# Optimization experiments

Hardware: AMD Instinct MI355X
Metric: run time of the kernel (lower is better)

Reference implementation:

```python
import jax, jax.numpy as jnp
import numpy as np

T, DM = 2048, 2048
H, KV, D = 16, 2, 128
E, I_MOE, I_SH = 16, 768, 768
TOP_K, N_GROUP, TOPK_GROUP = 4, 4, 2
ROPE_THETA = 1e6
EPS = 1e-5
ROUTED_SCALE = 1.0


def rmsnorm(x, w):
    v = jnp.mean(x * x, axis=-1, keepdims=True)
    return x * jax.lax.rsqrt(v + EPS) * w


def apply_rope(x, pos):
    # partial rotary: first D//2 dims rotated (neox style), rest passthrough
    rd = D // 2
    half = rd // 2
    inv = 1.0 / (ROPE_THETA ** (jnp.arange(0, rd, 2, dtype=jnp.float32) / rd))
    freqs = pos.astype(jnp.float32)[:, None] * inv  # [T, half]
    cos = jnp.cos(freqs)[:, None, :]
    sin = jnp.sin(freqs)[:, None, :]
    x1, x2 = x[..., :half], x[..., half:rd]
    rot = jnp.concatenate([x1 * cos - x2 * sin, x2 * cos + x1 * sin], axis=-1)
    return jnp.concatenate([rot, x[..., rd:]], axis=-1)


def mlp(x, wgu, wd):
    g, u = jnp.split(x @ wgu, 2, axis=-1)
    return (jax.nn.silu(g) * u) @ wd


def attention(x, pos, w_qkv, b_qkv, w_o, q_norm_w, k_norm_w):
    qkv = x @ w_qkv + b_qkv
    q, k, v = jnp.split(qkv, [H * D, H * D + KV * D], axis=-1)
    q = rmsnorm(q.reshape(T, H, D), q_norm_w)
    k = rmsnorm(k.reshape(T, KV, D), k_norm_w)
    v = v.reshape(T, KV, D)
    q = apply_rope(q, pos)
    k = apply_rope(k, pos)
    rep = H // KV
    k = jnp.repeat(k, rep, axis=1)
    v = jnp.repeat(v, rep, axis=1)
    scores = jnp.einsum('thd,shd->hts', q, k) * (D ** -0.5)
    causal = pos[:, None] >= pos[None, :]
    scores = jnp.where(causal[None], scores, jnp.finfo(scores.dtype).min)
    p = jax.nn.softmax(scores, axis=-1)
    o = jnp.einsum('hts,shd->thd', p, v).reshape(T, H * D)
    return o @ w_o


def moe(x, gate_w, gate_bias, shared_wgu, shared_wd, expert_wgu, expert_wd):
    # sigmoid grouped top-k routing with e_score_correction_bias (DeepSeek/GLM style)
    logits = x.astype(jnp.float32) @ gate_w
    scores = jax.nn.sigmoid(logits)
    sb = scores + gate_bias
    g = sb.reshape(T, N_GROUP, E // N_GROUP)
    group_scores = jnp.sum(jax.lax.top_k(g, 2)[0], axis=-1)  # [T, n_group]
    _, gi = jax.lax.top_k(group_scores, TOPK_GROUP)
    gmask = jnp.zeros((T, N_GROUP)).at[jnp.arange(T)[:, None], gi].set(1.0)
    emask = jnp.repeat(gmask, E // N_GROUP, axis=1)
    masked = jnp.where(emask > 0, sb, -jnp.inf)
    _, idx = jax.lax.top_k(masked, TOP_K)  # [T, top_k]
    w = jnp.take_along_axis(scores, idx, axis=1)
    w = w / jnp.sum(w, axis=1, keepdims=True)  # renormalize (norm_topk_prob)
    cw = jnp.zeros((T, E)).at[jnp.arange(T)[:, None], idx].add(w)  # dense combine weights
    gu = jnp.einsum('td,edi->tei', x, expert_wgu)  # [T, E, 2I]
    gt, ut = jnp.split(gu, 2, axis=-1)
    act = jax.nn.silu(gt) * ut * cw[:, :, None]
    routed = jnp.einsum('tei,eid->td', act, expert_wd)
    shared = mlp(x, shared_wgu, shared_wd)
    return routed * ROUTED_SCALE + shared


def setup_inputs() -> dict:
    key = jax.random.key(0)
    ks = jax.random.split(key, 12)
    s = 0.02
    return {
        'positions': jnp.arange(T, dtype=jnp.int32),
        'hidden_states': jax.random.normal(ks[0], (T, DM), jnp.float32),
        'residual': jax.random.normal(ks[1], (T, DM), jnp.float32),
        'ln1_w': jnp.ones((DM,), jnp.float32),
        'ln2_w': jnp.ones((DM,), jnp.float32),
        'w_qkv': jax.random.normal(ks[2], (DM, (H + 2 * KV) * D), jnp.float32) * s,
        'b_qkv': jnp.zeros(((H + 2 * KV) * D,), jnp.float32),
        'w_o': jax.random.normal(ks[3], (H * D, DM), jnp.float32) * s,
        'q_norm_w': jnp.ones((D,), jnp.float32),
        'k_norm_w': jnp.ones((D,), jnp.float32),
        'gate_w': jax.random.normal(ks[4], (DM, E), jnp.float32) * s,
        'gate_bias': jax.random.normal(ks[5], (E,), jnp.float32) * 0.1,
        'shared_wgu': jax.random.normal(ks[6], (DM, 2 * I_SH), jnp.float32) * s,
        'shared_wd': jax.random.normal(ks[7], (I_SH, DM), jnp.float32) * s,
        'expert_wgu': jax.random.normal(ks[8], (E, DM, 2 * I_MOE), jnp.float32) * s,
        'expert_wd': jax.random.normal(ks[9], (E, I_MOE, DM), jnp.float32) * s,
    }


def reference(positions, hidden_states, residual, ln1_w, ln2_w, w_qkv, b_qkv, w_o,
              q_norm_w, k_norm_w, gate_w, gate_bias, shared_wgu, shared_wd,
              expert_wgu, expert_wd):
    # fused add + RMSNorm (residual is not None path)
    residual = hidden_states + residual
    h = rmsnorm(residual, ln1_w)
    h = attention(h, positions, w_qkv, b_qkv, w_o, q_norm_w, k_norm_w)
    residual = h + residual
    h = rmsnorm(residual, ln2_w)
    h = moe(h, gate_w, gate_bias, shared_wgu, shared_wd, expert_wgu, expert_wd)
    return h, residual
```

## Files before the change

kernel.cpp:

```cpp
#include <hip/hip_runtime.h>
#include <stdint.h>
#include <math.h>

#define T_ 2048
#define DM 2048
#define NH 16
#define NKV 2
#define HD 128
#define QKVN 2560
#define NE 16
#define IM 768
#define ISH 768
#define MAXROWS 10240
#define ROWS_ALL 12288
#define NBLK 136
#define SM_SCALE 0.08838834764831845f

typedef __attribute__((ext_vector_type(8))) short short8;
typedef __attribute__((ext_vector_type(4))) float f32x4;

__device__ __forceinline__ float bf2f(unsigned short u){ return __uint_as_float(((unsigned int)u)<<16); }
__device__ __forceinline__ unsigned short f2bf(float f){
  unsigned int u = __float_as_uint(f);
  return (unsigned short)((u + 0x7FFFu + ((u>>16)&1u)) >> 16);
}
__device__ __forceinline__ void split2(float x, unsigned short& hi, unsigned short& lo){
  hi = f2bf(x);
  lo = f2bf(x - bf2f(hi));
}

__device__ __forceinline__ void gload16(const void* g, void* l){
  __builtin_amdgcn_global_load_lds((const __attribute__((address_space(1))) unsigned int*)g,
                                   (__attribute__((address_space(3))) unsigned int*)l, 16, 0, 0);
}

__device__ __forceinline__ int xcd_swz(int bid, int nwg){
  int q = nwg >> 3, r = nwg & 7, x = bid & 7, p = bid >> 3;
  return (x < r ? x*(q+1) : r*(q+1) + (x-r)*q) + p;
}

#define BAR()    asm volatile("s_barrier" ::: "memory")
#define VW(N)    asm volatile("s_waitcnt vmcnt(" #N ")" ::: "memory")
#define LW0()    do{ asm volatile("s_waitcnt lgkmcnt(0)" ::: "memory"); __builtin_amdgcn_sched_barrier(0); }while(0)

template<bool ILV>
__global__ void k_tconv(const float* __restrict__ src, unsigned short* __restrict__ dst,
                        const float* __restrict__ srcS, unsigned short* __restrict__ dstS,
                        int R, int C, size_t sS, size_t sD){
  int z = blockIdx.z;
  if (srcS && z == gridDim.z-1){ src = srcS; dst = dstS; }
  else { src += (size_t)z * sS; dst += (size_t)z * sD; }
  __shared__ float tile[64*65];
  int tid = threadIdx.x;
  int r0 = blockIdx.y*64, c0 = blockIdx.x*64;
  int lr = tid>>4, lc = (tid&15)*4;
  #pragma unroll
  for (int j=0;j<4;j++){
    int row = j*16 + lr;
    float4 v = *(const float4*)&src[(size_t)(r0+row)*C + c0 + lc];
    float* t = &tile[row*65 + lc];
    t[0]=v.x; t[1]=v.y; t[2]=v.z; t[3]=v.w;
  }
  __syncthreads();
  #pragma unroll
  for (int jj=0;jj<2;jj++){
    int slot = jj*256 + tid;
    int c = slot>>3, ro = (slot&7)*8;
    int cg = c0 + c;
    int cd = cg;
    if (ILV){ int b = cg>>3, inner = cg&7; cd = (b<96 ? b*16 : (b-96)*16+8) + inner; }
    short8 o;
    #pragma unroll
    for (int k=0;k<8;k++) o[k] = (short)f2bf(tile[(ro+k)*65 + c]);
    *(short8*)&dst[(size_t)cd*R + r0 + ro] = o;
  }
}

__global__ void k_tconv2(const float* __restrict__ srcA, unsigned short* __restrict__ dhiA,
                         unsigned short* __restrict__ dloA,
                         const float* __restrict__ srcB, unsigned short* __restrict__ dhiB,
                         unsigned short* __restrict__ dloB){
  const float* src; unsigned short* dhi; unsigned short* dlo; int R, C;
  if (blockIdx.z == 0){ src = srcA; dhi = dhiA; dlo = dloA; R = DM; C = QKVN; }
  else {
    if (blockIdx.x >= DM/64) return;
    src = srcB; dhi = dhiB; dlo = dloB; R = DM; C = DM;
  }
  __shared__ float tile[64*65];
  int tid = threadIdx.x;
  int r0 = blockIdx.y*64, c0 = blockIdx.x*64;
  int lr = tid>>4, lc = (tid&15)*4;
  #pragma unroll
  for (int j=0;j<4;j++){
    int row = j*16 + lr;
    float4 v = *(const float4*)&src[(size_t)(r0+row)*C + c0 + lc];
    float* t = &tile[row*65 + lc];
    t[0]=v.x; t[1]=v.y; t[2]=v.z; t[3]=v.w;
  }
  __syncthreads();
  #pragma unroll
  for (int jj=0;jj<2;jj++){
    int slot = jj*256 + tid;
    int c = slot>>3, ro = (slot&7)*8;
    short8 oh, ol;
    #pragma unroll
    for (int k=0;k<8;k++){
      unsigned short h_, l_;
      split2(tile[(ro+k)*65 + c], h_, l_);
      oh[k] = (short)h_; ol[k] = (short)l_;
    }
    size_t o = (size_t)(c0+c)*R + r0 + ro;
    *(short8*)&dhi[o] = oh;
    *(short8*)&dlo[o] = ol;
  }
}

template<bool ROUTE>
__global__ void k_add_rmsnorm(const float* __restrict__ a, const float* __restrict__ b,
                              const float* __restrict__ w, float* __restrict__ resout,
                              unsigned short* __restrict__ ohi, unsigned short* __restrict__ olo,
                              unsigned short* __restrict__ obf,
                              const float* __restrict__ gw, const float* __restrict__ gbias,
                              int* __restrict__ idx4, float* __restrict__ w4){
  int t = blockIdx.x, tid = threadIdx.x;
  const float4* a4 = (const float4*)(a + (size_t)t*DM);
  const float4* b4 = (const float4*)(b + (size_t)t*DM);
  float4 va = a4[tid], vb = b4[tid];
  float4 wa = a4[tid+256], wb = b4[tid+256];
  float4 v0, v1;
  v0.x=va.x+vb.x; v0.y=va.y+vb.y; v0.z=va.z+vb.z; v0.w=va.w+vb.w;
  v1.x=wa.x+wb.x; v1.y=wa.y+wb.y; v1.z=wa.z+wb.z; v1.w=wa.w+wb.w;
  float s = v0.x*v0.x+v0.y*v0.y+v0.z*v0.z+v0.w*v0.w
          + v1.x*v1.x+v1.y*v1.y+v1.z*v1.z+v1.w*v1.w;
  #pragma unroll
  for (int o=32;o;o>>=1) s += __shfl_xor(s,o);
  __shared__ float sm[4];
  if ((tid&63)==0) sm[tid>>6]=s;
  __syncthreads();
  s = sm[0]+sm[1]+sm[2]+sm[3];
  float rs = rsqrtf(s*(1.f/(float)DM) + 1e-5f);
  ((float4*)(resout + (size_t)t*DM))[tid] = v0;
  ((float4*)(resout + (size_t)t*DM))[tid+256] = v1;
  const float4* w4p_ = (const float4*)w;
  float4 w0 = w4p_[tid], w1 = w4p_[tid+256];
  float n[8] = { v0.x*rs*w0.x, v0.y*rs*w0.y, v0.z*rs*w0.z, v0.w*rs*w0.w,
                 v1.x*rs*w1.x, v1.y*rs*w1.y, v1.z*rs*w1.z, v1.w*rs*w1.w };
  if (ohi){
    ushort4 h0,h1,l0,l1;
    split2(n[0],h0.x,l0.x); split2(n[1],h0.y,l0.y); split2(n[2],h0.z,l0.z); split2(n[3],h0.w,l0.w);
    split2(n[4],h1.x,l1.x); split2(n[5],h1.y,l1.y); split2(n[6],h1.z,l1.z); split2(n[7],h1.w,l1.w);
    ((ushort4*)(ohi + (size_t)t*DM))[tid] = h0;
    ((ushort4*)(ohi + (size_t)t*DM))[tid+256] = h1;
    ((ushort4*)(olo + (size_t)t*DM))[tid] = l0;
    ((ushort4*)(olo + (size_t)t*DM))[tid+256] = l1;
  }
  if (obf){
    ushort4 o0 = make_ushort4(f2bf(n[0]),f2bf(n[1]),f2bf(n[2]),f2bf(n[3]));
    ushort4 o1 = make_ushort4(f2bf(n[4]),f2bf(n[5]),f2bf(n[6]),f2bf(n[7]));
    ((ushort4*)(obf + (size_t)t*DM))[tid] = o0;
    ((ushort4*)(obf + (size_t)t*DM))[tid+256] = o1;
  }
  if constexpr (ROUTE){
    __shared__ float xrow[DM];
    __shared__ float red[16][17];
    #pragma unroll
    for (int jj=0;jj<4;jj++) xrow[4*tid+jj] = n[jj];
    #pragma unroll
    for (int jj=0;jj<4;jj++) xrow[1024+4*tid+jj] = n[4+jj];
    __syncthreads();
    int e = tid & 15, grp = tid >> 4;
    float part = 0.f;
    #pragma unroll 8
    for (int c = grp; c < DM; c += 16)
      part += xrow[c] * gw[(size_t)c*16 + e];
    red[grp][e] = part;
    __syncthreads();
    if (tid==0){
      float sc[16], sb[16];
      for (int ee=0;ee<16;ee++){
        float lg = 0.f;
        for (int g2=0;g2<16;g2++) lg += red[g2][ee];
        sc[ee] = 1.f/(1.f+expf(-lg));
        sb[ee] = sc[ee] + gbias[ee];
      }
      float gs[4];
      for (int g=0;g<4;g++){
        float m1=-3.4e38f, m2=-3.4e38f;
        for (int j=0;j<4;j++){
          float v = sb[g*4+j];
          if (v>m1){ m2=m1; m1=v; } else if (v>m2) m2=v;
        }
        gs[g]=m1+m2;
      }
      int g1=0; for (int g=1;g<4;g++) if (gs[g]>gs[g1]) g1=g;
      int g2=-1; for (int g=0;g<4;g++){ if (g==g1) continue; if (g2<0 || gs[g]>gs[g2]) g2=g; }
      float msk[16];
      for (int ee=0;ee<16;ee++){ int g=ee>>2; msk[ee] = (g==g1||g==g2)? sb[ee] : -3.4e38f; }
      int id[4]; float wv[4]; float wsum=0.f;
      for (int s2=0;s2<4;s2++){
        int bb=0; float bv=-3.5e38f;
        for (int ee=0;ee<16;ee++) if (msk[ee]>bv){ bv=msk[ee]; bb=ee; }
        id[s2]=bb; wv[s2]=sc[bb]; wsum+=sc[bb]; msk[bb]=-3.5e38f;
      }
      float invs = 1.f/wsum;
      for (int s2=0;s2<4;s2++){
        idx4[t*4+s2]=id[s2];
        w4[t*4+s2]=wv[s2]*invs;
      }
    }
  }
}

template<bool GATHER, bool ACT>
__global__ __launch_bounds__(256) void k_gemm2(
    const unsigned short* __restrict__ A, const unsigned short* __restrict__ Be,
    const unsigned short* __restrict__ Bsh, unsigned short* __restrict__ C,
    int K, int lda, int ldb, int ldc,
    const int* __restrict__ offs, size_t sBe, const int* __restrict__ tok){
  int nx = gridDim.x;
  int nwg = nx * gridDim.y;
  int wid_ = xcd_swz(blockIdx.x + nx*blockIdx.y, nwg);
  int tN = wid_ % nx, tM = wid_ / nx;
  int rb = tM*128;
  if (rb >= offs[17]) return;
  const unsigned short* B;
  if (rb >= offs[16]) B = Bsh;
  else {
    int e=0;
    for (; e<15; ++e) if (offs[e+1] > rb) break;
    B = Be + (size_t)e*sBe;
  }
  __shared__ __align__(16) unsigned short As[2][4096];
  __shared__ __align__(16) unsigned short Bs[2][4096];
  int tid = threadIdx.x, lane = tid & 63, wwid = tid >> 6;
  int wr = wwid >> 1, wc = wwid & 1;
  const unsigned short* Bb = B + (size_t)tN*128*ldb;

  const unsigned short* Asrc0;
  const unsigned short* Asrc1;
  int r0s = tid>>2, r1s = r0s + 64;
  {
    if (GATHER){
      Asrc0 = A + (size_t)tok[rb + r0s]*lda;
      Asrc1 = A + (size_t)tok[rb + r1s]*lda;
    } else {
      Asrc0 = A + (size_t)(rb + r0s)*lda;
      Asrc1 = A + (size_t)(rb + r1s)*lda;
    }
  }
  int kc = tid&3;
  int sw = (r0s>>1)&3;
  int kcS = (kc ^ sw)*8;

  f32x4 acc[4][4];
  #pragma unroll
  for (int m=0;m<4;m++)
    #pragma unroll
    for (int n=0;n<4;n++) acc[m][n] = (f32x4){0.f,0.f,0.f,0.f};

  auto STAGE = [&](int b, int k0){
    gload16(Asrc0 + k0 + kcS, As[b] + (size_t)tid*8);
    gload16(Asrc1 + k0 + kcS, As[b] + (size_t)(256+tid)*8);
    gload16(Bb + (size_t)r0s*ldb + k0 + kcS, Bs[b] + (size_t)tid*8);
    gload16(Bb + (size_t)r1s*ldb + k0 + kcS, Bs[b] + (size_t)(256+tid)*8);
  };

  int nt = K >> 5, L = nt - 1;
  STAGE(0, 0);
  if (L >= 1) STAGE(1, 32);
  int i15 = lane & 15, g = lane >> 4;
  for (int i=0; i<nt; ++i){
    int cur = i & 1;
    if (i < L) { VW(4); } else { VW(0); }
    BAR();
    short8 af[4], bfr[4];
    #pragma unroll
    for (int m=0;m<4;m++){
      int row = wr*64 + m*16 + i15;
      int geff = g ^ ((row>>1)&3);
      af[m] = *(const short8*)(As[cur] + row*32 + geff*8);
    }
    #pragma unroll
    for (int n=0;n<4;n++){
      int row = wc*64 + n*16 + i15;
      int geff = g ^ ((row>>1)&3);
      bfr[n] = *(const short8*)(Bs[cur] + row*32 + geff*8);
    }
    LW0();
    BAR();
    if (i + 2 <= L) STAGE(cur, (i+2)*32);
    __builtin_amdgcn_s_setprio(1);
    #pragma unroll
    for (int m=0;m<4;m++)
      #pragma unroll
      for (int n=0;n<4;n++)
        acc[m][n] = __builtin_amdgcn_mfma_f32_16x16x32_bf16(af[m], bfr[n], acc[m][n], 0,0,0);
    __builtin_amdgcn_s_setprio(0);
  }

  if (ACT){
    int rbase = rb + wr*64, cb = tN*128 + wc*64;
    #pragma unroll
    for (int m=0;m<4;m++){
      int r0 = rbase + m*16 + ((lane>>4)<<2);
      #pragma unroll
      for (int n=0;n<4;n++){
        int f = ((cb + n*16)>>1) + (lane&7);
        #pragma unroll
        for (int r=0;r<4;r++){
          float v = acc[m][n][r];
          float vp = __shfl_xor(v, 8);
          if (!(lane&8)){
            float gg = v;
            float a = gg/(1.f+__expf(-gg))*vp;
            C[(size_t)(r0+r)*ldc + f] = f2bf(a);
          }
        }
      }
    }
  } else {
    int rbase = rb + wr*64, cb = tN*128 + wc*64;
    #pragma unroll
    for (int m=0;m<4;m++){
      int r0 = rbase + m*16 + ((lane>>4)<<2);
      #pragma unroll
      for (int n=0;n<4;n++){
        int c = cb + n*16 + (lane&15);
        #pragma unroll
        for (int r=0;r<4;r++) C[(size_t)(r0+r)*ldc + c] = f2bf(acc[m][n][r]);
      }
    }
  }
}

__global__ __launch_bounds__(256) void k_gemm_hp(
    const unsigned short* __restrict__ Ah, const unsigned short* __restrict__ Al,
    const unsigned short* __restrict__ Bh, const unsigned short* __restrict__ Bl,
    float* __restrict__ Cf,
    int K, int lda, int ldb, int ldc){
  int nx = gridDim.x, nwg = nx*gridDim.y;
  int w = xcd_swz(blockIdx.x + nx*blockIdx.y, nwg);
  int tN = w % nx, tM = w / nx;

  __shared__ __align__(16) unsigned short AsH[2][4096], AsL[2][4096];
  __shared__ __align__(16) unsigned short BsH[2][4096], BsL[2][4096];
  int tid = threadIdx.x, lane = tid & 63, wid = tid >> 6;
  int wr = wid >> 1, wc = wid & 1;
  const unsigned short* Abh = Ah + (size_t)tM*128*lda;
  const unsigned short* Abl = Al + (size_t)tM*128*lda;
  const unsigned short* Bbh = Bh + (size_t)tN*128*ldb;
  const unsigned short* Bbl = Bl + (size_t)tN*128*ldb;

  f32x4 acc[4][4];
  #pragma unroll
  for (int m=0;m<4;m++)
    #pragma unroll
    for (int n=0;n<4;n++) acc[m][n] = (f32x4){0.f,0.f,0.f,0.f};

  auto STAGE = [&](int b, int k0){
    #pragma unroll
    for (int j=0;j<2;j++){
      int cb = j*256 + tid;
      int row = cb>>2, kc = cb&3;
      int kcS = (kc ^ ((row>>1)&3))*8;
      size_t go = (size_t)row*lda + k0 + kcS;
      gload16(Abh + go, AsH[b] + (size_t)cb*8);
      gload16(Abl + go, AsL[b] + (size_t)cb*8);
      size_t bo = (size_t)row*ldb + k0 + kcS;
      gload16(Bbh + bo, BsH[b] + (size_t)cb*8);
      gload16(Bbl + bo, BsL[b] + (size_t)cb*8);
    }
  };

  int nt = K >> 5, L = nt - 1;
  STAGE(0, 0);
  if (L >= 1) STAGE(1, 32);
  int i15 = lane & 15, g = lane >> 4;
  for (int i=0; i<nt; ++i){
    int cur = i & 1;
    if (i < L) { VW(8); } else { VW(0); }
    BAR();
    short8 afh[4], afl[4], bfh[4], bfl[4];
    #pragma unroll
    for (int m=0;m<4;m++){
      int row = wr*64 + m*16 + i15;
      int ro = row*32 + (g ^ ((row>>1)&3))*8;
      afh[m] = *(const short8*)(AsH[cur] + ro);
      afl[m] = *(const short8*)(AsL[cur] + ro);
    }
    #pragma unroll
    for (int n=0;n<4;n++){
      int row = wc*64 + n*16 + i15;
      int ro = row*32 + (g ^ ((row>>1)&3))*8;
      bfh[n] = *(const short8*)(BsH[cur] + ro);
      bfl[n] = *(const short8*)(BsL[cur] + ro);
    }
    LW0();
    BAR();
    if (i + 2 <= L) STAGE(cur, (i+2)*32);
    __builtin_amdgcn_s_setprio(1);
    #pragma unroll
    for (int m=0;m<4;m++)
      #pragma unroll
      for (int n=0;n<4;n++){
        acc[m][n] = __builtin_amdgcn_mfma_f32_16x16x32_bf16(afh[m], bfh[n], acc[m][n], 0,0,0);
        acc[m][n] = __builtin_amdgcn_mfma_f32_16x16x32_bf16(afh[m], bfl[n], acc[m][n], 0,0,0);
        acc[m][n] = __builtin_amdgcn_mfma_f32_16x16x32_bf16(afl[m], bfh[n], acc[m][n], 0,0,0);
      }
    __builtin_amdgcn_s_setprio(0);
  }

  int rb = tM*128 + wr*64, cb = tN*128 + wc*64;
  #pragma unroll
  for (int m=0;m<4;m++){
    int r0 = rb + m*16 + ((lane>>4)<<2);
    #pragma unroll
    for (int n=0;n<4;n++){
      int c = cb + n*16 + (lane&15);
      #pragma unroll
      for (int r=0;r<4;r++) Cf[(size_t)(r0+r)*ldc + c] = acc[m][n][r];
    }
  }
}

__global__ __launch_bounds__(256) void k_qk_pers(
    const unsigned short* __restrict__ Qh, const unsigned short* __restrict__ Ql,
    const unsigned short* __restrict__ Kh, const unsigned short* __restrict__ Kl,
    float* __restrict__ Sp){
  int tM = blockIdx.x, z = blockIdx.y;
  int kvh = z >> 3;
  size_t tri = (size_t)tM*(tM+1)/2;
  const int ldq = NH*HD, ldk = NKV*HD;
  const unsigned short* Qbh = Qh + (size_t)(tM*128)*ldq + (size_t)z*HD;
  const unsigned short* Qbl = Ql + (size_t)(tM*128)*ldq + (size_t)z*HD;
  const unsigned short* Kbh = Kh + (size_t)kvh*HD;
  const unsigned short* Kbl = Kl + (size_t)kvh*HD;

  __shared__ __align__(16) unsigned short QsH[16384], QsL[16384];
  __shared__ __align__(16) unsigned short BsH[2][4096], BsL[2][4096];

  int tid = threadIdx.x, lane = tid & 63, wid = tid >> 6;
  int wr = wid >> 1, wc = wid & 1;
  int i15 = lane & 15, g = lane >> 4;

  #pragma unroll
  for (int j=0;j<8;j++){
    int gi = j*256 + tid;
    int chunk = gi >> 9;
    int row = (gi >> 2) & 127;
    int gg = gi & 3;
    int col = chunk*32 + (gg ^ ((row>>1)&3))*8;
    gload16(Qbh + (size_t)row*ldq + col, QsH + (size_t)gi*8);
    gload16(Qbl + (size_t)row*ldq + col, QsL + (size_t)gi*8);
  }

  auto BSTAGE = [&](int b, int ci){
    int tn = ci >> 2, c = ci & 3;
    const unsigned short* sh = Kbh + (size_t)(tn*128)*ldk;
    const unsigned short* sl = Kbl + (size_t)(tn*128)*ldk;
    #pragma unroll
    for (int j=0;j<2;j++){
      int gi = j*256 + tid;
      int row = gi >> 2, gg = gi & 3;
      int col = c*32 + (gg ^ ((row>>1)&3))*8;
      gload16(sh + (size_t)row*ldk + col, BsH[b] + (size_t)gi*8);
      gload16(sl + (size_t)row*ldk + col, BsL[b] + (size_t)gi*8);
    }
  };

  f32x4 acc[4][4];
  #pragma unroll
  for (int m=0;m<4;m++)
    #pragma unroll
    for (int n=0;n<4;n++) acc[m][n] = (f32x4){0.f,0.f,0.f,0.f};

  int NC = (tM+1)*4;
  BSTAGE(0, 0);
  BSTAGE(1, 1);
  for (int ci=0; ci<NC; ++ci){
    int cur = ci & 1, c = ci & 3, tn = ci >> 2;
    if (ci < NC-1) { VW(4); } else { VW(0); }
    BAR();
    short8 afh[4], afl[4], bfh[4], bfl[4];
    #pragma unroll
    for (int m=0;m<4;m++){
      int row = wr*64 + m*16 + i15;
      int ro = c*4096 + row*32 + (g ^ ((row>>1)&3))*8;
      afh[m] = *(const short8*)(QsH + ro);
      afl[m] = *(const short8*)(QsL + ro);
    }
    #pragma unroll
    for (int n=0;n<4;n++){
      int row = wc*64 + n*16 + i15;
      int ro = row*32 + (g ^ ((row>>1)&3))*8;
      bfh[n] = *(const short8*)(BsH[cur] + ro);
      bfl[n] = *(const short8*)(BsL[cur] + ro);
    }
    LW0();
    BAR();
    if (ci + 2 < NC) BSTAGE(cur, ci+2);
    __builtin_amdgcn_s_setprio(1);
    #pragma unroll
    for (int m=0;m<4;m++)
      #pragma unroll
      for (int n=0;n<4;n++){
        acc[m][n] = __builtin_amdgcn_mfma_f32_16x16x32_bf16(afh[m], bfh[n], acc[m][n], 0,0,0);
        acc[m][n] = __builtin_amdgcn_mfma_f32_16x16x32_bf16(afh[m], bfl[n], acc[m][n], 0,0,0);
        acc[m][n] = __builtin_amdgcn_mfma_f32_16x16x32_bf16(afl[m], bfh[n], acc[m][n], 0,0,0);
      }
    __builtin_amdgcn_s_setprio(0);
    if (c == 3){
      float* Cb = Sp + ((size_t)z*NBLK + tri + tn)*16384;
      #pragma unroll
      for (int m=0;m<4;m++){
        int r0 = wr*64 + m*16 + (g<<2);
        #pragma unroll
        for (int n=0;n<4;n++){
          int ccol = wc*64 + n*16 + i15;
          #pragma unroll
          for (int r=0;r<4;r++) Cb[(size_t)(r0+r)*128 + ccol] = acc[m][n][r];
        }
      }
      #pragma unroll
      for (int m=0;m<4;m++)
        #pragma unroll
        for (int n=0;n<4;n++) acc[m][n] = (f32x4){0.f,0.f,0.f,0.f};
    }
  }
}

__global__ __launch_bounds__(256) void k_pv_hp(
    const float* __restrict__ Sp,
    const unsigned short* __restrict__ Vh, const unsigned short* __restrict__ Vl,
    float* __restrict__ part, float* __restrict__ rsums){
  int c = blockIdx.x, tM = blockIdx.y, z = blockIdx.z;
  int kbeg = c*512;
  int kend = min((tM+1)*128, (c+1)*512);
  if (kbeg >= kend) return;
  int tMk = tM*128;
  size_t tri = (size_t)tM*(tM+1)/2;
  const float* Ab = Sp + ((size_t)z*NBLK + tri)*16384;
  const unsigned short* Bbh = Vh + (size_t)(z>>3)*HD*T_;
  const unsigned short* Bbl = Vl + (size_t)(z>>3)*HD*T_;

  __shared__ __align__(16) float Asf[2][4096];
  __shared__ __align__(16) unsigned short BsH[2][4096], BsL[2][4096];
  int tid = threadIdx.x, lane = tid & 63, wid = tid >> 6;
  int wr = wid >> 1, wc = wid & 1;
  int i15 = lane & 15, g2 = (lane>>4)*2;

  int r0s = tid>>2, r1s = r0s + 64;
  int kcB = ((tid&3) ^ ((r0s>>1)&3))*8;
  int rowA = tid>>3, gA = tid&7;

  f32x4 acc[4][4];
  #pragma unroll
  for (int m=0;m<4;m++)
    #pragma unroll
    for (int n=0;n<4;n++) acc[m][n] = (f32x4){0.f,0.f,0.f,0.f};
  float rsum[4] = {0.f,0.f,0.f,0.f};

  auto STAGE = [&](int b, int k0){
    #pragma unroll
    for (int j=0;j<4;j++){
      int r = j*32 + rowA;
      int gS = gA ^ (r & 7);
      size_t ga = (size_t)(k0>>7)*16384 + (size_t)r*128 + (k0&127) + gS*4;
      gload16(Ab + ga, Asf[b] + ((size_t)j*256 + tid)*4);
    }
    size_t bo0 = (size_t)r0s*T_ + k0 + kcB;
    size_t bo1 = (size_t)r1s*T_ + k0 + kcB;
    gload16(Bbh + bo0, BsH[b] + (size_t)tid*8);
    gload16(Bbh + bo1, BsH[b] + (size_t)(256+tid)*8);
    gload16(Bbl + bo0, BsL[b] + (size_t)tid*8);
    gload16(Bbl + bo1, BsL[b] + (size_t)(256+tid)*8);
  };

  int nt = (kend - kbeg) >> 5, L = nt - 1;
  STAGE(0, kbeg);
  if (L >= 1) STAGE(1, kbeg + 32);
  for (int i=0; i<nt; ++i){
    int cur = i & 1;
    int k0 = kbeg + i*32;
    if (i < L) { VW(8); } else { VW(0); }
    BAR();
    int diag = (k0 >= tMk);
    short8 afh[4], afl[4], bfh[4], bfl[4];
    #pragma unroll
    for (int m=0;m<4;m++){
      int r = wr*64 + m*16 + i15;
      int s0 = r*8 + ((g2  ) ^ (r&7));
      int s1 = r*8 + ((g2+1) ^ (r&7));
      f32x4 a0 = *(const f32x4*)(Asf[cur] + s0*4);
      f32x4 a1 = *(const f32x4*)(Asf[cur] + s1*4);
      float pv[8] = {a0[0],a0[1],a0[2],a0[3],a1[0],a1[1],a1[2],a1[3]};
      if (diag){
        int kb = k0 & 127;
        #pragma unroll
        for (int j=0;j<8;j++){
          int kl = kb + ((j<4) ? g2*4 + j : (g2+1)*4 + (j-4));
          if (kl > r) pv[j] = -3.0e38f;
        }
      }
      short8 h8, l8;
      #pragma unroll
      for (int j=0;j<8;j++){
        float p = __expf(pv[j]*SM_SCALE);
        rsum[m] += p;
        unsigned short hh, ll; split2(p, hh, ll);
        h8[j] = (short)hh; l8[j] = (short)ll;
      }
      afh[m] = h8; afl[m] = l8;
    }
    #pragma unroll
    for (int n=0;n<4;n++){
      int row = wc*64 + n*16 + i15;
      int ro = row*32 + ((lane>>4) ^ ((row>>1)&3))*8;
      bfh[n] = *(const short8*)(BsH[cur] + ro);
      bfl[n] = *(const short8*)(BsL[cur] + ro);
    }
    LW0();
    BAR();
    if (i + 2 <= L) STAGE(cur, kbeg + (i+2)*32);
    __builtin_amdgcn_s_setprio(1);
    #pragma unroll
    for (int m=0;m<4;m++)
      #pragma unroll
      for (int n=0;n<4;n++){
        acc[m][n] = __builtin_amdgcn_mfma_f32_16x16x32_bf16(afh[m], bfh[n], acc[m][n], 0,0,0);
        acc[m][n] = __builtin_amdgcn_mfma_f32_16x16x32_bf16(afh[m], bfl[n], acc[m][n], 0,0,0);
        acc[m][n] = __builtin_amdgcn_mfma_f32_16x16x32_bf16(afl[m], bfh[n], acc[m][n], 0,0,0);
      }
    __builtin_amdgcn_s_setprio(0);
  }

  #pragma unroll
  for (int m=0;m<4;m++){
    float v = rsum[m];
    v += __shfl_xor(v, 16);
    v += __shfl_xor(v, 32);
    if ((lane>>4)==0 && wc==0)
      rsums[((size_t)c*NH + z)*T_ + tMk + wr*64 + m*16 + i15] = v;
  }

  float* Cb = part + (size_t)c*T_*DM + (size_t)tMk*DM + (size_t)z*HD;
  #pragma unroll
  for (int m=0;m<4;m++){
    int r0 = wr*64 + m*16 + ((lane>>4)<<2);
    #pragma unroll
    for (int n=0;n<4;n++){
      int ccol = wc*64 + n*16 + (lane&15);
      #pragma unroll
      for (int r=0;r<4;r++) Cb[(size_t)(r0+r)*DM + ccol] = acc[m][n][r];
    }
  }
}

__global__ void k_pv_reduce(const float* __restrict__ part, const float* __restrict__ rsums,
                            unsigned short* __restrict__ aoh, unsigned short* __restrict__ aol){
  int t = blockIdx.x, tid = threadIdx.x;
  int nc = ((t>>7) + 4) >> 2;
  #pragma unroll
  for (int half=0; half<2; ++half){
    int idx = tid + half*256;
    int z = idx >> 5;
    float tot = 0.f;
    for (int c=0; c<nc; ++c) tot += rsums[((size_t)c*NH + z)*T_ + t];
    float inv = 1.f / tot;
    float4 s = ((const float4*)(part + (size_t)t*DM))[idx];
    for (int c=1; c<nc; ++c){
      float4 v = ((const float4*)(part + (size_t)c*T_*DM + (size_t)t*DM))[idx];
      s.x+=v.x; s.y+=v.y; s.z+=v.z; s.w+=v.w;
    }
    s.x*=inv; s.y*=inv; s.z*=inv; s.w*=inv;
    ushort4 h_, l_;
    split2(s.x,h_.x,l_.x); split2(s.y,h_.y,l_.y); split2(s.z,h_.z,l_.z); split2(s.w,h_.w,l_.w);
    ((ushort4*)(aoh + (size_t)t*DM))[idx] = h_;
    ((ushort4*)(aol + (size_t)t*DM))[idx] = l_;
  }
}

__global__ void k_qkv_post_hp(const float* __restrict__ qkv, const float* __restrict__ bias,
                              const float* __restrict__ qnw, const float* __restrict__ knw,
                              const int* __restrict__ pos_,
                              unsigned short* __restrict__ qhi, unsigned short* __restrict__ qlo,
                              unsigned short* __restrict__ khi, unsigned short* __restrict__ klo,
                              unsigned short* __restrict__ vThi, unsigned short* __restrict__ vTlo){
  int t = blockIdx.x;
  int half = threadIdx.x >> 7;
  int d = threadIdx.x & 127;
  int wseg = (threadIdx.x >> 6) & 1;
  float posf = (float)pos_[t];
  __shared__ float buf[2][128];
  __shared__ float ssum[2][2];
  __shared__ float inv_sh[32];
  if (threadIdx.x < 32)
    inv_sh[threadIdx.x] = (float)pow(1000000.0, -(double)threadIdx.x/32.0);
  __syncthreads();
  for (int it=0; it<10; ++it){
    int seg = it*2 + half;
    float x = qkv[(size_t)t*QKVN + seg*128 + d] + bias[seg*128 + d];
    float p = x*x;
    #pragma unroll
    for (int o=32;o;o>>=1) p += __shfl_xor(p,o);
    if ((threadIdx.x&63)==0) ssum[half][wseg] = p;
    __syncthreads();
    float rs = rsqrtf((ssum[half][0]+ssum[half][1])*(1.f/128.f) + 1e-5f);
    float w = (seg<16) ? qnw[d] : ((seg<18) ? knw[d] : 1.f);
    float nv = x*rs*w;
    buf[half][d] = nv;
    __syncthreads();
    float outv = (seg<18) ? nv : x;
    if (seg < 18 && d < 64){
      int i = d & 31;
      float ang = posf * inv_sh[i];
      float sn, cs; sincosf(ang, &sn, &cs);
      if (d < 32) outv = nv*cs - buf[half][d+32]*sn;
      else        outv = nv*cs + buf[half][d-32]*sn;
    }
    unsigned short h_, l_; split2(outv, h_, l_);
    if (seg < 16){ size_t o = ((size_t)t*NH + seg)*HD + d; qhi[o]=h_; qlo[o]=l_; }
    else if (seg < 18){ size_t o = ((size_t)t*NKV + (seg-16))*HD + d; khi[o]=h_; klo[o]=l_; }
    else { size_t o = ((size_t)(seg-18)*HD + d)*T_ + t; vThi[o]=h_; vTlo[o]=l_; }
    __syncthreads();
  }
}

__global__ void k_offplace(const int* __restrict__ idx4, int* __restrict__ offs,
                           int* __restrict__ rrow, int* __restrict__ tok){
  __shared__ int hist[16];
  __shared__ int hoff[16];
  __shared__ int fill[16];
  int tid = threadIdx.x;
  if (tid < 16) hist[tid] = 0;
  __syncthreads();
  for (int i = tid; i < ROWS_ALL; i += 256) tok[i] = 0;
  for (int i = tid; i < T_*4; i += 256)
    atomicAdd(&hist[idx4[i]], 1);
  __syncthreads();
  if (tid == 0){
    int o = 0;
    for (int e=0;e<16;e++){ hoff[e]=o; offs[e]=o; o += ((hist[e]+127)>>7)<<7; }
    offs[16]=o;
    offs[17]=o + T_;
  }
  if (tid < 16) fill[tid] = 0;
  __syncthreads();
  int off16 = offs[16];
  for (int t = tid; t < T_; t += 256){
    #pragma unroll
    for (int s=0;s<4;s++){
      int e = idx4[t*4+s];
      int p = atomicAdd(&fill[e],1);
      int r = hoff[e]+p;
      rrow[t*4+s]=r;
      tok[r]=t;
    }
    tok[off16+t] = t;
  }
}

__global__ void k_combine(const unsigned short* __restrict__ eout,
                          const int* __restrict__ rrow, const float* __restrict__ w4,
                          const int* __restrict__ offs, float* __restrict__ outh){
  int t = blockIdx.x;
  int rs = offs[16] + t;
  int r0=rrow[t*4+0], r1=rrow[t*4+1], r2=rrow[t*4+2], r3=rrow[t*4+3];
  float w0=w4[t*4+0], w1=w4[t*4+1], w2=w4[t*4+2], w3=w4[t*4+3];
  for (int d=threadIdx.x; d<DM; d+=256){
    float v = bf2f(eout[(size_t)rs*DM+d])
            + w0*bf2f(eout[(size_t)r0*DM+d]) + w1*bf2f(eout[(size_t)r1*DM+d])
            + w2*bf2f(eout[(size_t)r2*DM+d]) + w3*bf2f(eout[(size_t)r3*DM+d]);
    outh[(size_t)t*DM+d] = v;
  }
}

extern "C" void kernel_launch(void* const* d_in, const int* in_sizes, int n_in,
                              void* d_out, int out_size, void* d_ws, size_t ws_size,
                              hipStream_t stream){
  const int*   positions = (const int*)d_in[0];
  const float* hidden    = (const float*)d_in[1];
  const float* residual  = (const float*)d_in[2];
  const float* ln1       = (const float*)d_in[3];
  const float* ln2       = (const float*)d_in[4];
  const float* w_qkv     = (const float*)d_in[5];
  const float* b_qkv     = (const float*)d_in[6];
  const float* w_o       = (const float*)d_in[7];
  const float* qnw       = (const float*)d_in[8];
  const float* knw       = (const float*)d_in[9];
  const float* gate_w    = (const float*)d_in[10];
  const float* gate_b    = (const float*)d_in[11];
  const float* sh_wgu    = (const float*)d_in[12];
  const float* sh_wd     = (const float*)d_in[13];
  const float* e_wgu     = (const float*)d_in[14];
  const float* e_wd      = (const float*)d_in[15];
  float* out_h   = (float*)d_out;
  float* out_res = (float*)d_out + (size_t)T_*DM;

  char* ws = (char*)d_ws;
  size_t off = 0;
  auto alloc = [&](size_t b){ size_t r = off; off += (b + 255) & ~(size_t)255; return r; };

  size_t o_h2b  = alloc((size_t)T_*DM*2);
  size_t o_idx  = alloc((size_t)T_*4*4);
  size_t o_w4   = alloc((size_t)T_*4*4);
  size_t o_offs = alloc(72);
  size_t o_rrow = alloc((size_t)T_*4*4);
  size_t o_tok  = alloc((size_t)ROWS_ALL*4);

  size_t U0 = off;
  size_t a = U0;
  auto allocA = [&](size_t b){ size_t r = a; a += (b + 255) & ~(size_t)255; return r; };
  size_t o_h1h  = allocA((size_t)T_*DM*2);
  size_t o_h1l  = allocA((size_t)T_*DM*2);
  size_t o_wqh  = allocA((size_t)QKVN*DM*2);
  size_t o_wql  = allocA((size_t)QKVN*DM*2);
  size_t o_qkvf = allocA((size_t)T_*QKVN*4);
  size_t o_qh   = allocA((size_t)T_*NH*HD*2);
  size_t o_ql   = allocA((size_t)T_*NH*HD*2);
  size_t o_kh   = allocA((size_t)T_*NKV*HD*2);
  size_t o_kl   = allocA((size_t)T_*NKV*HD*2);
  size_t o_vth  = allocA((size_t)NKV*HD*T_*2);
  size_t o_vtl  = allocA((size_t)NKV*HD*T_*2);
  size_t o_woh  = allocA((size_t)DM*DM*2);
  size_t o_wol  = allocA((size_t)DM*DM*2);
  size_t o_aoh  = allocA((size_t)T_*DM*2);
  size_t o_aol  = allocA((size_t)T_*DM*2);
  size_t o_attnP= allocA((size_t)T_*DM*4);
  size_t o_rsum = allocA((size_t)4*NH*T_*4);
  size_t o_Sp   = allocA((size_t)NH*NBLK*16384*4);
  size_t o_pvp  = allocA((size_t)4*T_*DM*4);
  size_t b_ = U0;
  auto allocB = [&](size_t b){ size_t r = b_; b_ += (b + 255) & ~(size_t)255; return r; };
  size_t o_ewgu = allocB((size_t)NE*2*IM*DM*2);
  size_t o_ewd  = allocB((size_t)NE*DM*IM*2);
  size_t o_shgu = allocB((size_t)2*ISH*DM*2);
  size_t o_shwd = allocB((size_t)DM*ISH*2);
  size_t o_actx = allocB((size_t)ROWS_ALL*IM*2);
  size_t o_eout = allocB((size_t)ROWS_ALL*DM*2);

  unsigned short* h2b   = (unsigned short*)(ws+o_h2b);
  int*   idx4  = (int*)(ws+o_idx);
  float* w4p   = (float*)(ws+o_w4);
  int*   offs  = (int*)(ws+o_offs);
  int*   rrow  = (int*)(ws+o_rrow);
  int*   tok   = (int*)(ws+o_tok);
  unsigned short* h1h = (unsigned short*)(ws+o_h1h);
  unsigned short* h1l = (unsigned short*)(ws+o_h1l);
  unsigned short* wqh = (unsigned short*)(ws+o_wqh);
  unsigned short* wql = (unsigned short*)(ws+o_wql);
  float*          qkvf= (float*)(ws+o_qkvf);
  unsigned short* qh  = (unsigned short*)(ws+o_qh);
  unsigned short* ql  = (unsigned short*)(ws+o_ql);
  unsigned short* kh  = (unsigned short*)(ws+o_kh);
  unsigned short* kl  = (unsigned short*)(ws+o_kl);
  unsigned short* vth = (unsigned short*)(ws+o_vth);
  unsigned short* vtl = (unsigned short*)(ws+o_vtl);
  unsigned short* woh = (unsigned short*)(ws+o_woh);
  unsigned short* wol = (unsigned short*)(ws+o_wol);
  unsigned short* aoh = (unsigned short*)(ws+o_aoh);
  unsigned short* aol = (unsigned short*)(ws+o_aol);
  float*          attnP=(float*)(ws+o_attnP);
  float*          rsums=(float*)(ws+o_rsum);
  float*          Sp  = (float*)(ws+o_Sp);
  float*          pvpart = (float*)(ws+o_pvp);
  unsigned short* ewguT=(unsigned short*)(ws+o_ewgu);
  unsigned short* ewdT = (unsigned short*)(ws+o_ewd);
  unsigned short* shguT=(unsigned short*)(ws+o_shgu);
  unsigned short* shwdT=(unsigned short*)(ws+o_shwd);
  unsigned short* actx= (unsigned short*)(ws+o_actx);
  unsigned short* eout= (unsigned short*)(ws+o_eout);

  k_tconv2<<<dim3(QKVN/64, DM/64, 2),256,0,stream>>>(w_qkv, wqh, wql, w_o, woh, wol);

  k_add_rmsnorm<false><<<T_,256,0,stream>>>(hidden, residual, ln1, out_res, h1h, h1l, nullptr,
                                            nullptr, nullptr, nullptr, nullptr);

  k_gemm_hp<<<dim3(QKVN/128,T_/128,1),256,0,stream>>>(
      h1h, h1l, wqh, wql, qkvf, DM, DM, DM, QKVN);
  k_qkv_post_hp<<<T_,256,0,stream>>>(qkvf, b_qkv, qnw, knw, positions, qh, ql, kh, kl, vth, vtl);

  k_qk_pers<<<dim3(T_/128,NH),256,0,stream>>>(qh, ql, kh, kl, Sp);
  k_pv_hp<<<dim3(4,T_/128,NH),256,0,stream>>>(Sp, vth, vtl, pvpart, rsums);
  k_pv_reduce<<<T_,256,0,stream>>>(pvpart, rsums, aoh, aol);
  k_gemm_hp<<<dim3(DM/128,T_/128,1),256,0,stream>>>(
      aoh, aol, woh, wol, attnP, DM, DM, DM, DM);

  k_add_rmsnorm<true><<<T_,256,0,stream>>>(attnP, out_res, ln2, out_res, nullptr, nullptr, h2b,
                                           gate_w, gate_b, idx4, w4p);

  k_offplace<<<1,256,0,stream>>>(idx4, offs, rrow, tok);

  k_tconv<true ><<<dim3(2*IM/64, DM/64, NE+1),256,0,stream>>>(
      e_wgu, ewguT, sh_wgu, shguT, DM, 2*IM, (size_t)DM*2*IM, (size_t)2*IM*DM);
  k_tconv<false><<<dim3(DM/64, IM/64, NE+1),256,0,stream>>>(
      e_wd,  ewdT,  sh_wd,  shwdT, IM, DM,   (size_t)IM*DM,   (size_t)DM*IM);

  k_gemm2<true, true ><<<dim3(2*IM/128, ROWS_ALL/128, 1),256,0,stream>>>(
      h2b, ewguT, shguT, actx, DM, DM, DM, IM, offs, (size_t)2*IM*DM, tok);
  k_gemm2<false, false><<<dim3(DM/128, ROWS_ALL/128, 1),256,0,stream>>>(
      actx, ewdT, shwdT, eout, IM, IM, IM, DM, offs, (size_t)DM*IM, nullptr);

  k_combine<<<T_,256,0,stream>>>(eout, rrow, w4p, offs, out_h);
}
```

Baseline: 700.3 us.

## Balance causal QK^T tiles across a persistent grid of 256 blocks

Replaces the (row-tile, head) grid, where block work grew linearly with row index, with 256 persistent blocks that each take a contiguous run of 8 or 9 of the 2176 lower-triangular 128x128 score tiles. Each block reloads its Q tile only when the head or row tile changes and restarts the K double-buffer pipeline for each run. This targets the load imbalance and tail caused by triangular work per block, at the cost of extra Q reloads, pipeline restarts and a small serial search for the row index.

Measured after the change: 664.4 us. 5.1% less time.

```diff
diff --git a/kernel.cpp b/kernel.cpp
--- a/kernel.cpp
+++ b/kernel.cpp
@@ -427,14 +427,11 @@
     const unsigned short* __restrict__ Qh, const unsigned short* __restrict__ Ql,
     const unsigned short* __restrict__ Kh, const unsigned short* __restrict__ Kl,
     float* __restrict__ Sp){
-  int tM = blockIdx.x, z = blockIdx.y;
-  int kvh = z >> 3;
-  size_t tri = (size_t)tM*(tM+1)/2;
+  int bb = blockIdx.x;
+  int t0, ntile;
+  if (bb < 128){ t0 = bb*9; ntile = 9; }
+  else { t0 = 1152 + (bb-128)*8; ntile = 8; }
   const int ldq = NH*HD, ldk = NKV*HD;
-  const unsigned short* Qbh = Qh + (size_t)(tM*128)*ldq + (size_t)z*HD;
-  const unsigned short* Qbl = Ql + (size_t)(tM*128)*ldq + (size_t)z*HD;
-  const unsigned short* Kbh = Kh + (size_t)kvh*HD;
-  const unsigned short* Kbl = Kl + (size_t)kvh*HD;
 
   __shared__ __align__(16) unsigned short QsH[16384], QsL[16384];
   __shared__ __align__(16) unsigned short BsH[2][4096], BsL[2][4096];
@@ -443,89 +440,114 @@
   int wr = wid >> 1, wc = wid & 1;
   int i15 = lane & 15, g = lane >> 4;
 
-  #pragma unroll
-  for (int j=0;j<8;j++){
-    int gi = j*256 + tid;
-    int chunk = gi >> 9;
-    int row = (gi >> 2) & 127;
-    int gg = gi & 3;
-    int col = chunk*32 + (gg ^ ((row>>1)&3))*8;
-    gload16(Qbh + (size_t)row*ldq + col, QsH + (size_t)gi*8);
-    gload16(Qbl + (size_t)row*ldq + col, QsL + (size_t)gi*8);
-  }
-
-  auto BSTAGE = [&](int b, int ci){
-    int tn = ci >> 2, c = ci & 3;
-    const unsigned short* sh = Kbh + (size_t)(tn*128)*ldk;
-    const unsigned short* sl = Kbl + (size_t)(tn*128)*ldk;
-    #pragma unroll
-    for (int j=0;j<2;j++){
-      int gi = j*256 + tid;
-      int row = gi >> 2, gg = gi & 3;
-      int col = c*32 + (gg ^ ((row>>1)&3))*8;
-      gload16(sh + (size_t)row*ldk + col, BsH[b] + (size_t)gi*8);
-      gload16(sl + (size_t)row*ldk + col, BsL[b] + (size_t)gi*8);
-    }
-  };
-
   f32x4 acc[4][4];
   #pragma unroll
   for (int m=0;m<4;m++)
     #pragma unroll
     for (int n=0;n<4;n++) acc[m][n] = (f32x4){0.f,0.f,0.f,0.f};
 
-  int NC = (tM+1)*4;
-  BSTAGE(0, 0);
-  BSTAGE(1, 1);
-  for (int ci=0; ci<NC; ++ci){
-    int cur = ci & 1, c = ci & 3, tn = ci >> 2;
-    if (ci < NC-1) { VW(4); } else { VW(0); }
-    BAR();
-    short8 afh[4], afl[4], bfh[4], bfl[4];
-    #pragma unroll
-    for (int m=0;m<4;m++){
-      int row = wr*64 + m*16 + i15;
-      int ro = c*4096 + row*32 + (g ^ ((row>>1)&3))*8;
-      afh[m] = *(const short8*)(QsH + ro);
-      afl[m] = *(const short8*)(QsL + ro);
-    }
-    #pragma unroll
-    for (int n=0;n<4;n++){
-      int row = wc*64 + n*16 + i15;
-      int ro = row*32 + (g ^ ((row>>1)&3))*8;
-      bfh[n] = *(const short8*)(BsH[cur] + ro);
-      bfl[n] = *(const short8*)(BsL[cur] + ro);
-    }
-    LW0();
-    BAR();
-    if (ci + 2 < NC) BSTAGE(cur, ci+2);
-    __builtin_amdgcn_s_setprio(1);
-    #pragma unroll
-    for (int m=0;m<4;m++)
+  int curZ = -1, curM = -1;
+  const unsigned short* Kbh = Kh;
+  const unsigned short* Kbl = Kl;
+  int ti = 0;
+  while (ti < ntile){
+    int f = t0 + ti;
+    int z = f / 136;
+    int idx = f - z*136;
+    int tM = 0;
+    while ((tM+1)*(tM+2)/2 <= idx) tM++;
+    int tri = tM*(tM+1)/2;
+    int tnS = idx - tri;
+    int run = ntile - ti;
+    { int rem = tM+1 - tnS; if (rem < run) run = rem; }
+
+    if (z != curZ || tM != curM){
+      BAR();
+      const unsigned short* Qbh = Qh + (size_t)(tM*128)*ldq + (size_t)z*HD;
+      const unsigned short* Qbl = Ql + (size_t)(tM*128)*ldq + (size_t)z*HD;
+      #pragma unroll
+      for (int j=0;j<8;j++){
+        int gi = j*256 + tid;
+        int chunk = gi >> 9;
+        int row = (gi >> 2) & 127;
+        int gg = gi & 3;
+        int col = chunk*32 + (gg ^ ((row>>1)&3))*8;
+        gload16(Qbh + (size_t)row*ldq + col, QsH + (size_t)gi*8);
+        gload16(Qbl + (size_t)row*ldq + col, QsL + (size_t)gi*8);
+      }
+      curZ = z; curM = tM;
+      Kbh = Kh + (size_t)(z>>3)*HD;
+      Kbl = Kl + (size_t)(z>>3)*HD;
+    }
+
+    auto BSTAGE = [&](int b, int ci){
+      int tn = tnS + (ci >> 2), c = ci & 3;
+      const unsigned short* sh = Kbh + (size_t)(tn*128)*ldk;
+      const unsigned short* sl = Kbl + (size_t)(tn*128)*ldk;
+      #pragma unroll
+      for (int j=0;j<2;j++){
+        int gi = j*256 + tid;
+        int row = gi >> 2, gg = gi & 3;
+        int col = c*32 + (gg ^ ((row>>1)&3))*8;
+        gload16(sh + (size_t)row*ldk + col, BsH[b] + (size_t)gi*8);
+        gload16(sl + (size_t)row*ldk + col, BsL[b] + (size_t)gi*8);
+      }
+    };
+
+    int NC = run*4;
+    BSTAGE(0, 0);
+    BSTAGE(1, 1);
+    for (int ci=0; ci<NC; ++ci){
+      int cur = ci & 1, c = ci & 3, tn = tnS + (ci >> 2);
+      if (ci < NC-1) { VW(4); } else { VW(0); }
+      BAR();
+      short8 afh[4], afl[4], bfh[4], bfl[4];
+      #pragma unroll
+      for (int m=0;m<4;m++){
+        int row = wr*64 + m*16 + i15;
+        int ro = c*4096 + row*32 + (g ^ ((row>>1)&3))*8;
+        afh[m] = *(const short8*)(QsH + ro);
+        afl[m] = *(const short8*)(QsL + ro);
+      }
       #pragma unroll
       for (int n=0;n<4;n++){
-        acc[m][n] = __builtin_amdgcn_mfma_f32_16x16x32_bf16(afh[m], bfh[n], acc[m][n], 0,0,0);
-        acc[m][n] = __builtin_amdgcn_mfma_f32_16x16x32_bf16(afh[m], bfl[n], acc[m][n], 0,0,0);
-        acc[m][n] = __builtin_amdgcn_mfma_f32_16x16x32_bf16(afl[m], bfh[n], acc[m][n], 0,0,0);
-      }
-    __builtin_amdgcn_s_setprio(0);
-    if (c == 3){
-      float* Cb = Sp + ((size_t)z*NBLK + tri + tn)*16384;
-      #pragma unroll
-      for (int m=0;m<4;m++){
-        int r0 = wr*64 + m*16 + (g<<2);
+        int row = wc*64 + n*16 + i15;
+        int ro = row*32 + (g ^ ((row>>1)&3))*8;
+        bfh[n] = *(const short8*)(BsH[cur] + ro);
+        bfl[n] = *(const short8*)(BsL[cur] + ro);
+      }
+      LW0();
+      BAR();
+      if (ci + 2 < NC) BSTAGE(cur, ci+2);
+      __builtin_amdgcn_s_setprio(1);
+      #pragma unroll
+      for (int m=0;m<4;m++)
         #pragma unroll
         for (int n=0;n<4;n++){
-          int ccol = wc*64 + n*16 + i15;
+          acc[m][n] = __builtin_amdgcn_mfma_f32_16x16x32_bf16(afh[m], bfh[n], acc[m][n], 0,0,0);
+          acc[m][n] = __builtin_amdgcn_mfma_f32_16x16x32_bf16(afh[m], bfl[n], acc[m][n], 0,0,0);
+          acc[m][n] = __builtin_amdgcn_mfma_f32_16x16x32_bf16(afl[m], bfh[n], acc[m][n], 0,0,0);
+        }
+      __builtin_amdgcn_s_setprio(0);
+      if (c == 3){
+        float* Cb = Sp + ((size_t)z*NBLK + tri + tn)*16384;
+        #pragma unroll
+        for (int m=0;m<4;m++){
+          int r0 = wr*64 + m*16 + (g<<2);
           #pragma unroll
-          for (int r=0;r<4;r++) Cb[(size_t)(r0+r)*128 + ccol] = acc[m][n][r];
+          for (int n=0;n<4;n++){
+            int ccol = wc*64 + n*16 + i15;
+            #pragma unroll
+            for (int r=0;r<4;r++) Cb[(size_t)(r0+r)*128 + ccol] = acc[m][n][r];
+          }
         }
-      }
-      #pragma unroll
-      for (int m=0;m<4;m++)
         #pragma unroll
-        for (int n=0;n<4;n++) acc[m][n] = (f32x4){0.f,0.f,0.f,0.f};
-    }
+        for (int m=0;m<4;m++)
+          #pragma unroll
+          for (int n=0;n<4;n++) acc[m][n] = (f32x4){0.f,0.f,0.f,0.f};
+      }
+    }
+    ti += run;
   }
 }
 
@@ -880,7 +902,7 @@
       h1h, h1l, wqh, wql, qkvf, DM, DM, DM, QKVN);
   k_qkv_post_hp<<<T_,256,0,stream>>>(qkvf, b_qkv, qnw, knw, positions, qh, ql, kh, kl, vth, vtl);
 
-  k_qk_pers<<<dim3(T_/128,NH),256,0,stream>>>(qh, ql, kh, kl, Sp);
+  k_qk_pers<<<dim3(256),256,0,stream>>>(qh, ql, kh, kl, Sp);
   k_pv_hp<<<dim3(4,T_/128,NH),256,0,stream>>>(Sp, vth, vtl, pvpart, rsums);
   k_pv_reduce<<<T_,256,0,stream>>>(pvpart, rsums, aoh, aol);
   k_gemm_hp<<<dim3(DM/128,T_/128,1),256,0,stream>>>(
```
